# Kernel optimization log

Measured on AMD Instinct MI355X. Metric: run time of the kernel, lower is better.

Reference implementation:

```python
import jax, jax.numpy as jnp
import numpy as np

B, T, D = 2, 2048, 4096
H, G, d = 32, 8, 128
GROUP = H // G  # 4


def setup_inputs() -> dict:
    key = jax.random.key(0)
    ks = jax.random.split(key, 9)
    s = 0.02
    return {
        "hidden_states": jax.random.normal(ks[0], (B, T, D), jnp.float32),
        "Wq": jax.random.normal(ks[1], (D, D), jnp.float32) * s,
        "bq": jax.random.normal(ks[2], (D,), jnp.float32) * s,
        "Wk": jax.random.normal(ks[3], (G * d, D), jnp.float32) * s,
        "bk": jax.random.normal(ks[4], (G * d,), jnp.float32) * s,
        "Wv": jax.random.normal(ks[5], (G * d, D), jnp.float32) * s,
        "bv": jax.random.normal(ks[6], (G * d,), jnp.float32) * s,
        "Wo": jax.random.normal(ks[7], (D, D), jnp.float32) * s,
        "bo": jax.random.normal(ks[8], (D,), jnp.float32) * s,
    }


def reference(hidden_states, Wq, bq, Wk, bk, Wv, bv, Wo, bo):
    # projections (torch Linear: x @ W.T + b)
    q = hidden_states @ Wq.T + bq            # [B,T,D]
    k = hidden_states @ Wk.T + bk            # [B,T,G*d]
    v = hidden_states @ Wv.T + bv            # [B,T,G*d]

    # [B,G,group,T,d] for q; [B,G,T,d] for k,v. repeat_interleave(group, dim=1)
    # on [B,H,...] is exactly the (G, group) grouping of heads.
    q = q.reshape(B, T, G, GROUP, d).transpose(0, 2, 3, 1, 4)  # bgptd
    k = k.reshape(B, T, G, d).transpose(0, 2, 1, 3)            # bgsd
    v = v.reshape(B, T, G, d).transpose(0, 2, 1, 3)            # bgsd

    scale = 1.0 / np.sqrt(d).astype(np.float32)
    scores = jnp.einsum("bgptd,bgsd->bgpts", q, k) * scale     # [B,G,group,Tq,Tk]

    # causal additive mask: (j > i) * -1e9  (past_len = 0)
    i = jnp.arange(T)[:, None]
    j = jnp.arange(T)[None, :]
    causal_add = (j > i).astype(scores.dtype) * -1e9
    scores = scores + causal_add               # broadcast over b,g,p

    attn = jax.nn.softmax(scores, axis=-1)
    y = jnp.einsum("bgpts,bgsd->bgptd", attn, v)               # [B,G,group,T,d]
    y = y.transpose(0, 3, 1, 2, 4).reshape(B, T, D)            # [B,T,H*d]
    return y @ Wo.T + bo
```

## Files before the change

### kernel.cpp

```cpp
#include <hip/hip_runtime.h>
#include <hip/hip_bf16.h>
#include <cstdint>
#include <cstddef>

using bf16 = __hip_bfloat16;
typedef __attribute__((ext_vector_type(8))) short bf16x8;
typedef __attribute__((ext_vector_type(4))) float floatx4;

#define GLOBAL_AS __attribute__((address_space(1)))
#define LDS_AS    __attribute__((address_space(3)))

__device__ __forceinline__ void async_copy16(void* lds, const void* g) {
    __builtin_amdgcn_global_load_lds((GLOBAL_AS void*)(g), (LDS_AS void*)(lds), 16, 0, 0);
}

__device__ __forceinline__ floatx4 mfma_bf16(bf16x8 a, bf16x8 b, floatx4 c) {
    return __builtin_amdgcn_mfma_f32_16x16x32_bf16(a, b, c, 0, 0, 0);
}

__global__ void cvt_f32_bf16(const float* __restrict__ src, bf16* __restrict__ dst, int n) {
    int i = (blockIdx.x * blockDim.x + threadIdx.x) * 4;
    if (i < n) {
        float4 v = *(const float4*)(src + i);
        __align__(8) bf16 t[4];
        t[0] = __float2bfloat16(v.x);
        t[1] = __float2bfloat16(v.y);
        t[2] = __float2bfloat16(v.z);
        t[3] = __float2bfloat16(v.w);
        *(short4*)(dst + i) = *(const short4*)t;
    }
}

template <int OUTF>
__global__ __launch_bounds__(256, 3) void gemm_bt_bias(
    const bf16* __restrict__ A, const bf16* __restrict__ W,
    const float* __restrict__ bias, void* __restrict__ Cv,
    int M, int N, int K)
{
    __shared__ __align__(16) bf16 As[128 * 32];
    __shared__ __align__(16) bf16 Ws[128 * 32];

    const int tid  = threadIdx.x;
    const int lane = tid & 63;
    const int wave = tid >> 6;
    const int quad = lane >> 4;
    const int l16  = lane & 15;
    const int wm = (wave >> 1) * 64;
    const int wn = (wave & 1) * 64;

    const int bm = blockIdx.x;
    const int bn = blockIdx.y;

    floatx4 acc[4][4];
#pragma unroll
    for (int i = 0; i < 4; ++i)
#pragma unroll
        for (int j = 0; j < 4; ++j) acc[i][j] = (floatx4){0.f, 0.f, 0.f, 0.f};

    const int srow = tid >> 2;
    const int scol = (tid & 3) * 8;
    const bf16* gA = A + (size_t)(bm * 128 + srow) * K + scol;
    const bf16* gW = W + (size_t)(bn * 128 + srow) * K + scol;
    bf16* lA0 = As + tid * 8;
    bf16* lA1 = As + 2048 + tid * 8;
    bf16* lW0 = Ws + tid * 8;
    bf16* lW1 = Ws + 2048 + tid * 8;
    const size_t skip = (size_t)64 * K;

    const int kt_n = K >> 5;
    for (int kt = 0; kt < kt_n; ++kt) {
        __syncthreads();
        const bf16* ga = gA + kt * 32;
        const bf16* gw = gW + kt * 32;
        async_copy16(lA0, ga);
        async_copy16(lA1, ga + skip);
        async_copy16(lW0, gw);
        async_copy16(lW1, gw + skip);
        __syncthreads();

        bf16x8 af[4], bfr[4];
#pragma unroll
        for (int mi = 0; mi < 4; ++mi)
            af[mi] = *(const bf16x8*)(As + (wm + mi * 16 + l16) * 32 + quad * 8);
#pragma unroll
        for (int ni = 0; ni < 4; ++ni)
            bfr[ni] = *(const bf16x8*)(Ws + (wn + ni * 16 + l16) * 32 + quad * 8);
#pragma unroll
        for (int mi = 0; mi < 4; ++mi)
#pragma unroll
            for (int ni = 0; ni < 4; ++ni)
                acc[mi][ni] = mfma_bf16(af[mi], bfr[ni], acc[mi][ni]);
    }

#pragma unroll
    for (int mi = 0; mi < 4; ++mi) {
        const int row0 = bm * 128 + wm + mi * 16 + quad * 4;
#pragma unroll
        for (int ni = 0; ni < 4; ++ni) {
            const int col = bn * 128 + wn + ni * 16 + l16;
            const float bv = bias[col];
            if (OUTF) {
                float* C = (float*)Cv;
#pragma unroll
                for (int r = 0; r < 4; ++r)
                    C[(size_t)(row0 + r) * N + col] = acc[mi][ni][r] + bv;
            } else {
                bf16* C = (bf16*)Cv;
#pragma unroll
                for (int r = 0; r < 4; ++r)
                    C[(size_t)(row0 + r) * N + col] = __float2bfloat16(acc[mi][ni][r] + bv);
            }
        }
    }
}

__global__ __launch_bounds__(256, 3) void gemm_kv(
    const bf16* __restrict__ A,
    const bf16* __restrict__ Wk, const bf16* __restrict__ Wv,
    const float* __restrict__ bk, const float* __restrict__ bv,
    bf16* __restrict__ kout, bf16* __restrict__ vt,
    int M, int K)
{
    __shared__ __align__(16) bf16 As[128 * 32];
    __shared__ __align__(16) bf16 Ws[128 * 32];

    const int tid  = threadIdx.x;
    const int lane = tid & 63;
    const int wave = tid >> 6;
    const int quad = lane >> 4;
    const int l16  = lane & 15;
    const int wm = (wave >> 1) * 64;
    const int wn = (wave & 1) * 64;

    const int bm = blockIdx.x;
    const int bn = blockIdx.y;
    const bool isK = (bn < 8);
    const int nb = isK ? bn : (bn - 8);
    const bf16* Wsel  = isK ? Wk : Wv;
    const float* bsel = isK ? bk : bv;

    floatx4 acc[4][4];
#pragma unroll
    for (int i = 0; i < 4; ++i)
#pragma unroll
        for (int j = 0; j < 4; ++j) acc[i][j] = (floatx4){0.f, 0.f, 0.f, 0.f};

    const int srow = tid >> 2;
    const int scol = (tid & 3) * 8;
    const bf16* gA = A    + (size_t)(bm * 128 + srow) * K + scol;
    const bf16* gW = Wsel + (size_t)(nb * 128 + srow) * K + scol;
    bf16* lA0 = As + tid * 8;
    bf16* lA1 = As + 2048 + tid * 8;
    bf16* lW0 = Ws + tid * 8;
    bf16* lW1 = Ws + 2048 + tid * 8;
    const size_t skip = (size_t)64 * K;

    const int kt_n = K >> 5;
    for (int kt = 0; kt < kt_n; ++kt) {
        __syncthreads();
        const bf16* ga = gA + kt * 32;
        const bf16* gw = gW + kt * 32;
        async_copy16(lA0, ga);
        async_copy16(lA1, ga + skip);
        async_copy16(lW0, gw);
        async_copy16(lW1, gw + skip);
        __syncthreads();

        bf16x8 af[4], bfr[4];
#pragma unroll
        for (int mi = 0; mi < 4; ++mi)
            af[mi] = *(const bf16x8*)(As + (wm + mi * 16 + l16) * 32 + quad * 8);
#pragma unroll
        for (int ni = 0; ni < 4; ++ni)
            bfr[ni] = *(const bf16x8*)(Ws + (wn + ni * 16 + l16) * 32 + quad * 8);
#pragma unroll
        for (int mi = 0; mi < 4; ++mi)
#pragma unroll
            for (int ni = 0; ni < 4; ++ni)
                acc[mi][ni] = mfma_bf16(af[mi], bfr[ni], acc[mi][ni]);
    }

#pragma unroll
    for (int mi = 0; mi < 4; ++mi) {
        const int row0 = bm * 128 + wm + mi * 16 + quad * 4;
#pragma unroll
        for (int ni = 0; ni < 4; ++ni) {
            const int col = nb * 128 + wn + ni * 16 + l16;
            const float bvv = bsel[col];
            if (isK) {
#pragma unroll
                for (int r = 0; r < 4; ++r)
                    kout[(size_t)(row0 + r) * 1024 + col] = __float2bfloat16(acc[mi][ni][r] + bvv);
            } else {
                __align__(8) bf16 tmp[4];
#pragma unroll
                for (int r = 0; r < 4; ++r) tmp[r] = __float2bfloat16(acc[mi][ni][r] + bvv);
                const int b  = row0 >> 11;
                const int t0 = row0 & 2047;
                bf16* dst = vt + ((size_t)(b * 1024 + col)) * 2048 + t0;
                *(short4*)dst = *(const short4*)tmp;
            }
        }
    }
}

__global__ __launch_bounds__(256, 2) void attn_fwd(
    const bf16* __restrict__ qb, const bf16* __restrict__ kb,
    const bf16* __restrict__ vtb, bf16* __restrict__ ob)
{
    constexpr int T  = 2048;
    constexpr int DQ = 4096;
    constexpr int DK = 1024;

    __shared__ __align__(16) bf16 Ks[2][64 * 128];
    __shared__ __align__(16) bf16 Vs[2][128 * 64];
    __shared__ __align__(16) bf16 Ps[4][16][72];

    const int tid  = threadIdx.x;
    const int lane = tid & 63;
    const int wave = tid >> 6;
    const int quad = lane >> 4;
    const int l16  = lane & 15;
    const int swz  = l16 & 7;

    const int qi = blockIdx.x;
    const int bh = blockIdx.y;
    const int b  = bh >> 5;
    const int h  = bh & 31;
    const int g  = h >> 2;
    const int qtB = 31 - qi;
    const int qtA = qi;
    const int q0B = qtB * 64;
    const int q0A = qtA * 64;
    const int qw = wave * 16;

    const bf16* Qg = qb  + (size_t)b * T * DQ + (size_t)h * 128;
    const bf16* Kg = kb  + (size_t)b * T * DK + (size_t)g * 128;
    const bf16* Vg = vtb + ((size_t)b * DK + g * 128) * T;
    bf16*       Og = ob  + (size_t)b * T * DQ + (size_t)h * 128;

    bf16x8 qf[2][4];
    {
        const size_t rB = (size_t)(q0B + qw + l16) * DQ;
        const size_t rA = (size_t)(q0A + qw + l16) * DQ;
#pragma unroll
        for (int kk = 0; kk < 4; ++kk) {
            qf[0][kk] = *(const bf16x8*)(Qg + rB + kk * 32 + quad * 8);
            qf[1][kk] = *(const bf16x8*)(Qg + rA + kk * 32 + quad * 8);
        }
    }

    const int krow_l = tid >> 4;
    const int kc16   = tid & 15;
    const int vrow_l = tid >> 3;
    const int vc16   = tid & 7;

    auto STAGE = [&](int st_, int bi_) {
        const int s0_ = st_ * 64;
        bf16* kbp = &Ks[bi_][0];
        bf16* vbp = &Vs[bi_][0];
#pragma unroll
        for (int i = 0; i < 4; ++i) {
            const int r = i * 16 + krow_l;
            async_copy16(kbp + (i * 256 + tid) * 8,
                         Kg + (size_t)(s0_ + r) * DK + ((kc16 ^ (r & 7)) * 8));
        }
#pragma unroll
        for (int i = 0; i < 4; ++i) {
            const int r = i * 32 + vrow_l;
            async_copy16(vbp + (i * 256 + tid) * 8,
                         Vg + (size_t)r * T + s0_ + ((vc16 ^ (r & 7)) * 8));
        }
    };

    floatx4 oacc[2][8];
#pragma unroll
    for (int t = 0; t < 2; ++t)
#pragma unroll
        for (int i = 0; i < 8; ++i) oacc[t][i] = (floatx4){0.f, 0.f, 0.f, 0.f};
    float m_run[2][4], l_run[2][4];
#pragma unroll
    for (int t = 0; t < 2; ++t)
#pragma unroll
        for (int r = 0; r < 4; ++r) { m_run[t][r] = -1e30f; l_run[t][r] = 0.f; }

    const float scale = 0.08838834764831845f;

    STAGE(0, 0);
    __syncthreads();

    for (int st = 0; st <= qtB; ++st) {
        const int bi = st & 1;
        const int s0 = st * 64;

        if (st < qtB) STAGE(st + 1, bi ^ 1);

        const bf16* Kb = &Ks[bi][0];
        const bf16* Vb = &Vs[bi][0];

        const int ntile = (st <= qtA) ? 2 : 1;
#pragma unroll
        for (int t = 0; t < 2; ++t) {
            if (t >= ntile) break;
            const int q0t  = t ? q0A : q0B;
            const int qt_t = t ? qtA : qtB;

            floatx4 sacc[4];
#pragma unroll
            for (int i = 0; i < 4; ++i) sacc[i] = (floatx4){0.f, 0.f, 0.f, 0.f};
#pragma unroll
            for (int kk = 0; kk < 4; ++kk) {
                const int koff = ((kk * 4 + quad) ^ swz) * 8;
#pragma unroll
                for (int ni = 0; ni < 4; ++ni) {
                    bf16x8 bk8 = *(const bf16x8*)(Kb + (ni * 16 + l16) * 128 + koff);
                    sacc[ni] = mfma_bf16(qf[t][kk], bk8, sacc[ni]);
                }
            }

            const bool diag = (st == qt_t);
#pragma unroll
            for (int r = 0; r < 4; ++r) {
                const int qg = q0t + qw + quad * 4 + r;
                float sv[4];
#pragma unroll
                for (int ni = 0; ni < 4; ++ni) {
                    float x = sacc[ni][r] * scale;
                    if (diag && (s0 + ni * 16 + l16) > qg) x = -1e30f;
                    sv[ni] = x;
                }
                float mx = fmaxf(fmaxf(sv[0], sv[1]), fmaxf(sv[2], sv[3]));
                mx = fmaxf(mx, __shfl_xor(mx, 1, 64));
                mx = fmaxf(mx, __shfl_xor(mx, 2, 64));
                mx = fmaxf(mx, __shfl_xor(mx, 4, 64));
                mx = fmaxf(mx, __shfl_xor(mx, 8, 64));
                const float mnew  = fmaxf(m_run[t][r], mx);
                const float alpha = __expf(m_run[t][r] - mnew);
                float ssum = 0.f;
#pragma unroll
                for (int ni = 0; ni < 4; ++ni) {
                    float p = __expf(sv[ni] - mnew);
                    ssum += p;
                    Ps[wave][quad * 4 + r][ni * 16 + l16] = __float2bfloat16(p);
                }
                ssum += __shfl_xor(ssum, 1, 64);
                ssum += __shfl_xor(ssum, 2, 64);
                ssum += __shfl_xor(ssum, 4, 64);
                ssum += __shfl_xor(ssum, 8, 64);
                l_run[t][r] = l_run[t][r] * alpha + ssum;
                m_run[t][r] = mnew;
#pragma unroll
                for (int db = 0; db < 8; ++db) oacc[t][db][r] *= alpha;
            }
            asm volatile("s_waitcnt lgkmcnt(0)" ::: "memory");

#pragma unroll
            for (int kk = 0; kk < 2; ++kk) {
                bf16x8 ap = *(const bf16x8*)&Ps[wave][l16][kk * 32 + quad * 8];
                const int voff = ((kk * 4 + quad) ^ swz) * 8;
#pragma unroll
                for (int db = 0; db < 8; ++db) {
                    bf16x8 bv8 = *(const bf16x8*)(Vb + (db * 16 + l16) * 64 + voff);
                    oacc[t][db] = mfma_bf16(ap, bv8, oacc[t][db]);
                }
            }
        }

        __syncthreads();
    }

#pragma unroll
    for (int t = 0; t < 2; ++t) {
        const int q0t = t ? q0A : q0B;
#pragma unroll
        for (int r = 0; r < 4; ++r) {
            const float inv = 1.0f / l_run[t][r];
            const int qg = q0t + qw + quad * 4 + r;
#pragma unroll
            for (int db = 0; db < 8; ++db)
                Og[(size_t)qg * DQ + db * 16 + l16] = __float2bfloat16(oacc[t][db][r] * inv);
        }
    }
}

extern "C" void kernel_launch(void* const* d_in, const int* in_sizes, int n_in,
                              void* d_out, int out_size, void* d_ws, size_t ws_size,
                              hipStream_t stream)
{
    const float* hs = (const float*)d_in[0];
    const float* Wq = (const float*)d_in[1];
    const float* bq = (const float*)d_in[2];
    const float* Wk = (const float*)d_in[3];
    const float* bk = (const float*)d_in[4];
    const float* Wv = (const float*)d_in[5];
    const float* bv = (const float*)d_in[6];
    const float* Wo = (const float*)d_in[7];
    const float* bo = (const float*)d_in[8];
    float* out = (float*)d_out;

    const int M  = 4096;
    const int D  = 4096;
    const int DK = 1024;
    const size_t SZ_D  = (size_t)M * D;
    const size_t SZ_K  = (size_t)M * DK;

    bf16* hsb  = (bf16*)d_ws;
    bf16* Wqb  = hsb  + SZ_D;
    bf16* Wkb  = Wqb  + SZ_D;
    bf16* Wvb  = Wkb  + SZ_K;
    bf16* Wob  = Wvb  + SZ_K;
    bf16* q_buf = Wob + SZ_D;
    bf16* k_buf = q_buf + SZ_D;
    bf16* vt_buf = Wqb;
    bf16* o_buf  = hsb;

    dim3 blk(256);
    const int CB = 256;
    cvt_f32_bf16<<<(int)(SZ_D / 4 + CB - 1) / CB, CB, 0, stream>>>(hs, hsb, (int)SZ_D);
    cvt_f32_bf16<<<(int)(SZ_D / 4 + CB - 1) / CB, CB, 0, stream>>>(Wq, Wqb, (int)SZ_D);
    cvt_f32_bf16<<<(int)(SZ_K / 4 + CB - 1) / CB, CB, 0, stream>>>(Wk, Wkb, (int)SZ_K);
    cvt_f32_bf16<<<(int)(SZ_K / 4 + CB - 1) / CB, CB, 0, stream>>>(Wv, Wvb, (int)SZ_K);
    cvt_f32_bf16<<<(int)(SZ_D / 4 + CB - 1) / CB, CB, 0, stream>>>(Wo, Wob, (int)SZ_D);

    gemm_bt_bias<0><<<dim3(M / 128, D / 128), blk, 0, stream>>>(hsb, Wqb, bq, q_buf, M, D, D);
    gemm_kv<<<dim3(M / 128, 16), blk, 0, stream>>>(hsb, Wkb, Wvb, bk, bv, k_buf, vt_buf, M, D);
    attn_fwd<<<dim3(16, 64), blk, 0, stream>>>(q_buf, k_buf, vt_buf, o_buf);
    gemm_bt_bias<1><<<dim3(M / 128, D / 128), blk, 0, stream>>>(o_buf, Wob, bo, out, M, D, D);
}
```

Before: 791.1 us.

## Fold softmax scale into Q projection, add lazy rescale and MFMA priority hints

The attention scale is now applied in the Q projection epilogue, so the per-score multiply in attention goes away. The online softmax skips the running-max update and the rescale of the output accumulator when the whole wave's new max stays within 8 of the old one. This is the lazy-rescaling trick; it relies on fp32 headroom and costs a wave-wide vote plus branch divergence. s_setprio hints are placed around the two MFMA blocks to favour matrix issue over other waves.

After: 844.5 us. 6.7% more time.

```diff
diff --git a/kernel.cpp b/kernel.cpp
--- a/kernel.cpp
+++ b/kernel.cpp
@@ -35,7 +35,7 @@
 __global__ __launch_bounds__(256, 3) void gemm_bt_bias(
     const bf16* __restrict__ A, const bf16* __restrict__ W,
     const float* __restrict__ bias, void* __restrict__ Cv,
-    int M, int N, int K)
+    int M, int N, int K, float cscale)
 {
     __shared__ __align__(16) bf16 As[128 * 32];
     __shared__ __align__(16) bf16 Ws[128 * 32];
@@ -103,12 +103,12 @@
                 float* C = (float*)Cv;
 #pragma unroll
                 for (int r = 0; r < 4; ++r)
-                    C[(size_t)(row0 + r) * N + col] = acc[mi][ni][r] + bv;
+                    C[(size_t)(row0 + r) * N + col] = (acc[mi][ni][r] + bv) * cscale;
             } else {
                 bf16* C = (bf16*)Cv;
 #pragma unroll
                 for (int r = 0; r < 4; ++r)
-                    C[(size_t)(row0 + r) * N + col] = __float2bfloat16(acc[mi][ni][r] + bv);
+                    C[(size_t)(row0 + r) * N + col] = __float2bfloat16((acc[mi][ni][r] + bv) * cscale);
             }
         }
     }
@@ -284,8 +284,6 @@
 #pragma unroll
         for (int r = 0; r < 4; ++r) { m_run[t][r] = -1e30f; l_run[t][r] = 0.f; }
 
-    const float scale = 0.08838834764831845f;
-
     STAGE(0, 0);
     __syncthreads();
 
@@ -308,6 +306,7 @@
             floatx4 sacc[4];
 #pragma unroll
             for (int i = 0; i < 4; ++i) sacc[i] = (floatx4){0.f, 0.f, 0.f, 0.f};
+            __builtin_amdgcn_s_setprio(1);
 #pragma unroll
             for (int kk = 0; kk < 4; ++kk) {
                 const int koff = ((kk * 4 + quad) ^ swz) * 8;
@@ -317,6 +316,7 @@
                     sacc[ni] = mfma_bf16(qf[t][kk], bk8, sacc[ni]);
                 }
             }
+            __builtin_amdgcn_s_setprio(0);
 
             const bool diag = (st == qt_t);
 #pragma unroll
@@ -325,7 +325,7 @@
                 float sv[4];
 #pragma unroll
                 for (int ni = 0; ni < 4; ++ni) {
-                    float x = sacc[ni][r] * scale;
+                    float x = sacc[ni][r];
                     if (diag && (s0 + ni * 16 + l16) > qg) x = -1e30f;
                     sv[ni] = x;
                 }
@@ -334,26 +334,42 @@
                 mx = fmaxf(mx, __shfl_xor(mx, 2, 64));
                 mx = fmaxf(mx, __shfl_xor(mx, 4, 64));
                 mx = fmaxf(mx, __shfl_xor(mx, 8, 64));
-                const float mnew  = fmaxf(m_run[t][r], mx);
-                const float alpha = __expf(m_run[t][r] - mnew);
+                const float mold = m_run[t][r];
                 float ssum = 0.f;
-#pragma unroll
-                for (int ni = 0; ni < 4; ++ni) {
-                    float p = __expf(sv[ni] - mnew);
-                    ssum += p;
-                    Ps[wave][quad * 4 + r][ni * 16 + l16] = __float2bfloat16(p);
+                if (__all(mx <= mold + 8.0f)) {
+#pragma unroll
+                    for (int ni = 0; ni < 4; ++ni) {
+                        float p = __expf(sv[ni] - mold);
+                        ssum += p;
+                        Ps[wave][quad * 4 + r][ni * 16 + l16] = __float2bfloat16(p);
+                    }
+                    ssum += __shfl_xor(ssum, 1, 64);
+                    ssum += __shfl_xor(ssum, 2, 64);
+                    ssum += __shfl_xor(ssum, 4, 64);
+                    ssum += __shfl_xor(ssum, 8, 64);
+                    l_run[t][r] += ssum;
+                } else {
+                    const float mnew  = fmaxf(mold, mx);
+                    const float alpha = __expf(mold - mnew);
+#pragma unroll
+                    for (int ni = 0; ni < 4; ++ni) {
+                        float p = __expf(sv[ni] - mnew);
+                        ssum += p;
+                        Ps[wave][quad * 4 + r][ni * 16 + l16] = __float2bfloat16(p);
+                    }
+                    ssum += __shfl_xor(ssum, 1, 64);
+                    ssum += __shfl_xor(ssum, 2, 64);
+                    ssum += __shfl_xor(ssum, 4, 64);
+                    ssum += __shfl_xor(ssum, 8, 64);
+                    l_run[t][r] = l_run[t][r] * alpha + ssum;
+                    m_run[t][r] = mnew;
+#pragma unroll
+                    for (int db = 0; db < 8; ++db) oacc[t][db][r] *= alpha;
                 }
-                ssum += __shfl_xor(ssum, 1, 64);
-                ssum += __shfl_xor(ssum, 2, 64);
-                ssum += __shfl_xor(ssum, 4, 64);
-                ssum += __shfl_xor(ssum, 8, 64);
-                l_run[t][r] = l_run[t][r] * alpha + ssum;
-                m_run[t][r] = mnew;
-#pragma unroll
-                for (int db = 0; db < 8; ++db) oacc[t][db][r] *= alpha;
             }
             asm volatile("s_waitcnt lgkmcnt(0)" ::: "memory");
 
+            __builtin_amdgcn_s_setprio(1);
 #pragma unroll
             for (int kk = 0; kk < 2; ++kk) {
                 bf16x8 ap = *(const bf16x8*)&Ps[wave][l16][kk * 32 + quad * 8];
@@ -364,6 +380,7 @@
                     oacc[t][db] = mfma_bf16(ap, bv8, oacc[t][db]);
                 }
             }
+            __builtin_amdgcn_s_setprio(0);
         }
 
         __syncthreads();
@@ -422,8 +439,9 @@
     cvt_f32_bf16<<<(int)(SZ_K / 4 + CB - 1) / CB, CB, 0, stream>>>(Wv, Wvb, (int)SZ_K);
     cvt_f32_bf16<<<(int)(SZ_D / 4 + CB - 1) / CB, CB, 0, stream>>>(Wo, Wob, (int)SZ_D);
 
-    gemm_bt_bias<0><<<dim3(M / 128, D / 128), blk, 0, stream>>>(hsb, Wqb, bq, q_buf, M, D, D);
+    const float scale = 0.08838834764831845f;
+    gemm_bt_bias<0><<<dim3(M / 128, D / 128), blk, 0, stream>>>(hsb, Wqb, bq, q_buf, M, D, D, scale);
     gemm_kv<<<dim3(M / 128, 16), blk, 0, stream>>>(hsb, Wkb, Wvb, bk, bv, k_buf, vt_buf, M, D);
     attn_fwd<<<dim3(16, 64), blk, 0, stream>>>(q_buf, k_buf, vt_buf, o_buf);
-    gemm_bt_bias<1><<<dim3(M / 128, D / 128), blk, 0, stream>>>(o_buf, Wob, bo, out, M, D, D);
-}
+    gemm_bt_bias<1><<<dim3(M / 128, D / 128), blk, 0, stream>>>(o_buf, Wob, bo, out, M, D, D, 1.0f);
+}
```

## Compute transposed scores in attention and fold softmax scale into Q projection

Applied to the files above, without the earlier changes.

The QK^T MFMA now swaps its operands, so each lane holds a single query row across key columns. The softmax max and sum reductions therefore need only two cross-lane shuffles instead of four per row, running statistics become one scalar per tile, and P is written to LDS as packed 4-element stores. The 1/sqrt(d) scale is applied in the Q projection epilogue, which removes the per-element multiply from attention. The cost is extra shuffles to redistribute alpha and 1/l to the output-accumulator layout, plus a small precision change from scaling before the bf16 rounding of Q.

Result: faster. 767.9 us (-2.9%).

```diff
diff --git a/kernel.cpp b/kernel.cpp
--- a/kernel.cpp
+++ b/kernel.cpp
@@ -35,7 +35,7 @@
 __global__ __launch_bounds__(256, 3) void gemm_bt_bias(
     const bf16* __restrict__ A, const bf16* __restrict__ W,
     const float* __restrict__ bias, void* __restrict__ Cv,
-    int M, int N, int K)
+    int M, int N, int K, float cscale)
 {
     __shared__ __align__(16) bf16 As[128 * 32];
     __shared__ __align__(16) bf16 Ws[128 * 32];
@@ -103,12 +103,12 @@
                 float* C = (float*)Cv;
 #pragma unroll
                 for (int r = 0; r < 4; ++r)
-                    C[(size_t)(row0 + r) * N + col] = acc[mi][ni][r] + bv;
+                    C[(size_t)(row0 + r) * N + col] = (acc[mi][ni][r] + bv) * cscale;
             } else {
                 bf16* C = (bf16*)Cv;
 #pragma unroll
                 for (int r = 0; r < 4; ++r)
-                    C[(size_t)(row0 + r) * N + col] = __float2bfloat16(acc[mi][ni][r] + bv);
+                    C[(size_t)(row0 + r) * N + col] = __float2bfloat16((acc[mi][ni][r] + bv) * cscale);
             }
         }
     }
@@ -278,13 +278,11 @@
     for (int t = 0; t < 2; ++t)
 #pragma unroll
         for (int i = 0; i < 8; ++i) oacc[t][i] = (floatx4){0.f, 0.f, 0.f, 0.f};
-    float m_run[2][4], l_run[2][4];
-#pragma unroll
-    for (int t = 0; t < 2; ++t)
-#pragma unroll
-        for (int r = 0; r < 4; ++r) { m_run[t][r] = -1e30f; l_run[t][r] = 0.f; }
-
-    const float scale = 0.08838834764831845f;
+    float m_run[2], l_run[2];
+#pragma unroll
+    for (int t = 0; t < 2; ++t) { m_run[t] = -1e30f; l_run[t] = 0.f; }
+
+    const int bsrc = (lane & 48) + quad * 4;
 
     STAGE(0, 0);
     __syncthreads();
@@ -311,47 +309,63 @@
 #pragma unroll
             for (int kk = 0; kk < 4; ++kk) {
                 const int koff = ((kk * 4 + quad) ^ swz) * 8;
+                const bf16x8 qv = qf[t][kk];
 #pragma unroll
                 for (int ni = 0; ni < 4; ++ni) {
-                    bf16x8 bk8 = *(const bf16x8*)(Kb + (ni * 16 + l16) * 128 + koff);
-                    sacc[ni] = mfma_bf16(qf[t][kk], bk8, sacc[ni]);
+                    bf16x8 kf = *(const bf16x8*)(Kb + (ni * 16 + l16) * 128 + koff);
+                    sacc[ni] = mfma_bf16(kf, qv, sacc[ni]);
                 }
             }
 
             const bool diag = (st == qt_t);
-#pragma unroll
-            for (int r = 0; r < 4; ++r) {
-                const int qg = q0t + qw + quad * 4 + r;
-                float sv[4];
-#pragma unroll
-                for (int ni = 0; ni < 4; ++ni) {
-                    float x = sacc[ni][r] * scale;
-                    if (diag && (s0 + ni * 16 + l16) > qg) x = -1e30f;
-                    sv[ni] = x;
+            const int qg = q0t + qw + l16;
+            float sv[4][4];
+#pragma unroll
+            for (int ni = 0; ni < 4; ++ni)
+#pragma unroll
+                for (int r = 0; r < 4; ++r) {
+                    float x = sacc[ni][r];
+                    if (diag && (s0 + ni * 16 + quad * 4 + r) > qg) x = -1e30f;
+                    sv[ni][r] = x;
                 }
-                float mx = fmaxf(fmaxf(sv[0], sv[1]), fmaxf(sv[2], sv[3]));
-                mx = fmaxf(mx, __shfl_xor(mx, 1, 64));
-                mx = fmaxf(mx, __shfl_xor(mx, 2, 64));
-                mx = fmaxf(mx, __shfl_xor(mx, 4, 64));
-                mx = fmaxf(mx, __shfl_xor(mx, 8, 64));
-                const float mnew  = fmaxf(m_run[t][r], mx);
-                const float alpha = __expf(m_run[t][r] - mnew);
-                float ssum = 0.f;
-#pragma unroll
-                for (int ni = 0; ni < 4; ++ni) {
-                    float p = __expf(sv[ni] - mnew);
+
+            float pm[4];
+#pragma unroll
+            for (int ni = 0; ni < 4; ++ni)
+                pm[ni] = fmaxf(fmaxf(sv[ni][0], sv[ni][1]), fmaxf(sv[ni][2], sv[ni][3]));
+            float mx = fmaxf(fmaxf(pm[0], pm[1]), fmaxf(pm[2], pm[3]));
+            mx = fmaxf(mx, __shfl_xor(mx, 16, 64));
+            mx = fmaxf(mx, __shfl_xor(mx, 32, 64));
+
+            const float mold  = m_run[t];
+            const float mnew  = fmaxf(mold, mx);
+            const float alpha = __expf(mold - mnew);
+            m_run[t] = mnew;
+
+            float ssum = 0.f;
+#pragma unroll
+            for (int ni = 0; ni < 4; ++ni) {
+                __align__(8) bf16 pb[4];
+#pragma unroll
+                for (int r = 0; r < 4; ++r) {
+                    float p = __expf(sv[ni][r] - mnew);
                     ssum += p;
-                    Ps[wave][quad * 4 + r][ni * 16 + l16] = __float2bfloat16(p);
+                    pb[r] = __float2bfloat16(p);
                 }
-                ssum += __shfl_xor(ssum, 1, 64);
-                ssum += __shfl_xor(ssum, 2, 64);
-                ssum += __shfl_xor(ssum, 4, 64);
-                ssum += __shfl_xor(ssum, 8, 64);
-                l_run[t][r] = l_run[t][r] * alpha + ssum;
-                m_run[t][r] = mnew;
-#pragma unroll
-                for (int db = 0; db < 8; ++db) oacc[t][db][r] *= alpha;
+                *(short4*)&Ps[wave][l16][ni * 16 + quad * 4] = *(const short4*)pb;
             }
+            ssum += __shfl_xor(ssum, 16, 64);
+            ssum += __shfl_xor(ssum, 32, 64);
+            l_run[t] = l_run[t] * alpha + ssum;
+
+            float ar[4];
+#pragma unroll
+            for (int r = 0; r < 4; ++r) ar[r] = __shfl(alpha, bsrc + r, 64);
+#pragma unroll
+            for (int db = 0; db < 8; ++db)
+#pragma unroll
+                for (int r = 0; r < 4; ++r) oacc[t][db][r] *= ar[r];
+
             asm volatile("s_waitcnt lgkmcnt(0)" ::: "memory");
 
 #pragma unroll
@@ -372,13 +386,16 @@
 #pragma unroll
     for (int t = 0; t < 2; ++t) {
         const int q0t = t ? q0A : q0B;
+        const float linv = 1.0f / l_run[t];
+        float ir[4];
+#pragma unroll
+        for (int r = 0; r < 4; ++r) ir[r] = __shfl(linv, bsrc + r, 64);
 #pragma unroll
         for (int r = 0; r < 4; ++r) {
-            const float inv = 1.0f / l_run[t][r];
             const int qg = q0t + qw + quad * 4 + r;
 #pragma unroll
             for (int db = 0; db < 8; ++db)
-                Og[(size_t)qg * DQ + db * 16 + l16] = __float2bfloat16(oacc[t][db][r] * inv);
+                Og[(size_t)qg * DQ + db * 16 + l16] = __float2bfloat16(oacc[t][db][r] * ir[r]);
         }
     }
 }
@@ -422,8 +439,9 @@
     cvt_f32_bf16<<<(int)(SZ_K / 4 + CB - 1) / CB, CB, 0, stream>>>(Wv, Wvb, (int)SZ_K);
     cvt_f32_bf16<<<(int)(SZ_D / 4 + CB - 1) / CB, CB, 0, stream>>>(Wo, Wob, (int)SZ_D);
 
-    gemm_bt_bias<0><<<dim3(M / 128, D / 128), blk, 0, stream>>>(hsb, Wqb, bq, q_buf, M, D, D);
+    const float scale = 0.08838834764831845f;
+    gemm_bt_bias<0><<<dim3(M / 128, D / 128), blk, 0, stream>>>(hsb, Wqb, bq, q_buf, M, D, D, scale);
     gemm_kv<<<dim3(M / 128, 16), blk, 0, stream>>>(hsb, Wkb, Wvb, bk, bv, k_buf, vt_buf, M, D);
     attn_fwd<<<dim3(16, 64), blk, 0, stream>>>(q_buf, k_buf, vt_buf, o_buf);
-    gemm_bt_bias<1><<<dim3(M / 128, D / 128), blk, 0, stream>>>(o_buf, Wob, bo, out, M, D, D);
-}
+    gemm_bt_bias<1><<<dim3(M / 128, D / 128), blk, 0, stream>>>(o_buf, Wob, bo, out, M, D, D, 1.0f);
+}
```
